# Kernel tuning notes

Hardware: AMD Instinct MI355X
Metric: run time of the kernel (lower is better)

Reference implementation:

```python
import jax, jax.numpy as jnp
import numpy as np

# --- HairBundle model constants (from init_kwargs: params + force_params) ---
# Nadrowski/Martin-style hair-bundle model with 5 state variables:
#   x_hb (bundle position), x_a (adaptation motor), p_m, p_gs, p_t (Ca probs)
LAM    = 1.0    # bundle friction
LAM_A  = 10.0   # adaptation-motor friction
K_GS   = 0.75   # gating-spring stiffness
K_SP   = 0.6    # stereociliary-pivot stiffness
K_ES   = 0.45   # extent spring stiffness
D_GATE = 0.5    # gating swing
DELTA  = 0.25   # channel sensitivity length
F_MAX  = 0.35   # max motor force
S_CA   = 0.9    # Ca feedback strength on motors
C_M    = 1.2    # Ca binding rate (motor site)
K_M    = 0.8    # Ca unbinding rate (motor site)
TAU_M  = 1.0
C_GS   = 0.7    # Ca binding rate (gating-spring site)
K_GSR  = 0.5    # Ca unbinding rate (gating-spring site)
TAU_GS = 1.0
C_T    = 0.3    # Ca binding rate (transduction site)
K_T    = 0.4    # Ca unbinding rate (transduction site)
TAU_T  = 1.0
HB_NOISE = 0.05 # diffusion on x_hb
A_NOISE  = 0.02 # diffusion on x_a
# force_params: sinusoidal driving force
F_AMP   = 0.5
F_OMEGA = 6.283185307179586
F_PHASE = 0.0

BATCH = 8_000_000  # number of SDE sample paths
NVARS = 5


def setup_inputs() -> dict:
    key = jax.random.key(0)
    k1, k2 = jax.random.split(key)
    t = jax.random.uniform(k1, (1,), dtype=jnp.float32)
    x = jax.random.normal(k2, (BATCH, NVARS), dtype=jnp.float32)
    return {"t": t, "x": x}


def reference(t, x):
    """Vectorized drift f(t, x) of the hair-bundle SDE (replaces the
    per-row python loop + sympy lambdified scalar evaluation) plus the
    constant diagonal diffusion g(t, x). Returns (drift, diffusion)."""
    x_hb, x_a, p_m, p_gs, p_t = (x[..., 0], x[..., 1], x[..., 2], x[..., 3], x[..., 4])

    # channel open probability and gating-spring force (elementwise, fused)
    p_o = jax.nn.sigmoid((x_hb - x_a) / DELTA)          # [B]
    f_gs = K_GS * (x_hb - x_a - D_GATE * p_o)           # [B]

    force = F_AMP * jnp.sin(F_OMEGA * t[0] + F_PHASE)   # scalar sin drive, added to dx_hb

    dx_hb = (-f_gs - K_SP * x_hb) / LAM + force
    dx_a  = (f_gs - K_ES * x_a - F_MAX * (1.0 - S_CA * p_m)) / LAM_A
    dp_m  = (C_M * p_o * (1.0 - p_m) - K_M * p_m) / TAU_M
    dp_gs = (C_GS * p_o * (1.0 - p_gs) - K_GSR * p_gs) / TAU_GS
    dp_t  = (C_T * p_o * (1.0 - p_t) - K_T * p_t) / TAU_T

    drift = jnp.stack([dx_hb, dx_a, dp_m, dp_gs, dp_t], axis=-1)  # [B, 5]

    # g: constant per-variable noise amplitudes tiled over the batch
    dsigma = jnp.array([HB_NOISE, A_NOISE, 0.0, 0.0, 0.0], dtype=x.dtype)
    diffusion = jnp.broadcast_to(dsigma, x.shape)  # [B, 5]

    return drift, diffusion
```

## Files before the change

### kernel.cpp

```cpp
#include <hip/hip_runtime.h>
#include <math.h>


__global__ __launch_bounds__(256) void hb_sde_kernel(
    const float* __restrict__ t,
    const float* __restrict__ x,
    float* __restrict__ out,
    int n_groups,
    long long batch)
{
    const long long tid = (long long)blockIdx.x * blockDim.x + threadIdx.x;
    if (tid >= n_groups) return;

    const float force = 0.5f * sinf(6.283185307179586f * t[0] + 0.0f);

    const float4* __restrict__ xv = (const float4*)x + tid * 5;
    float in[20];
    ((float4*)in)[0] = xv[0];
    ((float4*)in)[1] = xv[1];
    ((float4*)in)[2] = xv[2];
    ((float4*)in)[3] = xv[3];
    ((float4*)in)[4] = xv[4];

    float o[20];
#pragma unroll
    for (int r = 0; r < 4; ++r) {
        const float x_hb = in[r*5+0];
        const float x_a  = in[r*5+1];
        const float p_m  = in[r*5+2];
        const float p_gs = in[r*5+3];
        const float p_t  = in[r*5+4];

        const float p_o  = 1.0f / (1.0f + __expf(-4.0f * (x_hb - x_a)));
        const float f_gs = 0.75f * (x_hb - x_a - 0.5f * p_o);

        o[r*5+0] = -f_gs - 0.6f * x_hb + force;
        o[r*5+1] = 0.1f * (f_gs - 0.45f * x_a - 0.35f * (1.0f - 0.9f * p_m));
        o[r*5+2] = 1.2f * p_o * (1.0f - p_m)  - 0.8f * p_m;
        o[r*5+3] = 0.7f * p_o * (1.0f - p_gs) - 0.5f * p_gs;
        o[r*5+4] = 0.3f * p_o * (1.0f - p_t)  - 0.4f * p_t;
    }

    float4* __restrict__ dv = (float4*)out + tid * 5;
    dv[0] = ((float4*)o)[0];
    dv[1] = ((float4*)o)[1];
    dv[2] = ((float4*)o)[2];
    dv[3] = ((float4*)o)[3];
    dv[4] = ((float4*)o)[4];

    float4* __restrict__ gv = (float4*)(out + batch * 5) + tid * 5;
    gv[0] = make_float4(0.05f, 0.02f, 0.0f,  0.0f);
    gv[1] = make_float4(0.0f,  0.05f, 0.02f, 0.0f);
    gv[2] = make_float4(0.0f,  0.0f,  0.05f, 0.02f);
    gv[3] = make_float4(0.0f,  0.0f,  0.0f,  0.05f);
    gv[4] = make_float4(0.02f, 0.0f,  0.0f,  0.0f);
}

extern "C" void kernel_launch(void* const* d_in, const int* in_sizes, int n_in,
                              void* d_out, int out_size, void* d_ws, size_t ws_size,
                              hipStream_t stream) {
    const float* t = (const float*)d_in[0];
    const float* x = (const float*)d_in[1];
    float* out = (float*)d_out;

    const long long batch = (long long)in_sizes[1] / 5;
    const int n_groups = (int)(batch / 4);

    const int block = 256;
    const int grid = (n_groups + block - 1) / block;
    hb_sde_kernel<<<grid, block, 0, stream>>>(t, x, out, n_groups, batch);
}
```

Baseline: 456.5 us.

## Stage rows through LDS for coalesced float4 loads and nontemporal stores

Each block cooperatively loads 512 rows as contiguous float4s into shared memory, computes the drift in place, then writes drift and the constant diffusion pattern back with coalesced nontemporal stores. This replaces per-thread 80-byte-strided vector accesses that poorly coalesce. It adds LDS traffic and two barriers, uses smaller blocks, and drops the tail bounds check, assuming batch is a multiple of 512.

```diff
diff --git a/kernel.cpp b/kernel.cpp
--- a/kernel.cpp
+++ b/kernel.cpp
@@ -2,58 +2,70 @@
 #include <math.h>
 
 
-__global__ __launch_bounds__(256) void hb_sde_kernel(
+typedef float f4 __attribute__((ext_vector_type(4)));
+
+#define THREADS        128
+#define ROWS_PER_BLOCK 512
+#define F4_PER_BLOCK   (ROWS_PER_BLOCK * 5 / 4)
+#define F4_PER_THREAD  (F4_PER_BLOCK / THREADS)
+#define ROWS_PER_THREAD (ROWS_PER_BLOCK / THREADS)
+
+__global__ __launch_bounds__(THREADS) void hb_sde_kernel(
     const float* __restrict__ t,
     const float* __restrict__ x,
-    float* __restrict__ out,
-    int n_groups,
-    long long batch)
+    float* __restrict__ drift,
+    float* __restrict__ diff)
 {
-    const long long tid = (long long)blockIdx.x * blockDim.x + threadIdx.x;
-    if (tid >= n_groups) return;
+    __shared__ float lds[ROWS_PER_BLOCK * 5];
 
-    const float force = 0.5f * sinf(6.283185307179586f * t[0] + 0.0f);
+    const int i = threadIdx.x;
+    const long long f4base = (long long)blockIdx.x * F4_PER_BLOCK;
 
-    const float4* __restrict__ xv = (const float4*)x + tid * 5;
-    float in[20];
-    ((float4*)in)[0] = xv[0];
-    ((float4*)in)[1] = xv[1];
-    ((float4*)in)[2] = xv[2];
-    ((float4*)in)[3] = xv[3];
-    ((float4*)in)[4] = xv[4];
+    const float force = 0.5f * sinf(6.283185307179586f * t[0]);
 
-    float o[20];
+    const f4* __restrict__ xv = (const f4*)x + f4base;
+    f4* lv = (f4*)lds;
 #pragma unroll
-    for (int r = 0; r < 4; ++r) {
-        const float x_hb = in[r*5+0];
-        const float x_a  = in[r*5+1];
-        const float p_m  = in[r*5+2];
-        const float p_gs = in[r*5+3];
-        const float p_t  = in[r*5+4];
+    for (int k = 0; k < F4_PER_THREAD; ++k)
+        lv[i + k * THREADS] = __builtin_nontemporal_load(&xv[i + k * THREADS]);
+    __syncthreads();
+
+#pragma unroll
+    for (int r = 0; r < ROWS_PER_THREAD; ++r) {
+        const int o = (i * ROWS_PER_THREAD + r) * 5;
+        const float x_hb = lds[o + 0];
+        const float x_a  = lds[o + 1];
+        const float p_m  = lds[o + 2];
+        const float p_gs = lds[o + 3];
+        const float p_t  = lds[o + 4];
 
         const float p_o  = 1.0f / (1.0f + __expf(-4.0f * (x_hb - x_a)));
         const float f_gs = 0.75f * (x_hb - x_a - 0.5f * p_o);
 
-        o[r*5+0] = -f_gs - 0.6f * x_hb + force;
-        o[r*5+1] = 0.1f * (f_gs - 0.45f * x_a - 0.35f * (1.0f - 0.9f * p_m));
-        o[r*5+2] = 1.2f * p_o * (1.0f - p_m)  - 0.8f * p_m;
-        o[r*5+3] = 0.7f * p_o * (1.0f - p_gs) - 0.5f * p_gs;
-        o[r*5+4] = 0.3f * p_o * (1.0f - p_t)  - 0.4f * p_t;
+        lds[o + 0] = -f_gs - 0.6f * x_hb + force;
+        lds[o + 1] = 0.1f * (f_gs - 0.45f * x_a - 0.35f * (1.0f - 0.9f * p_m));
+        lds[o + 2] = 1.2f * p_o * (1.0f - p_m)  - 0.8f * p_m;
+        lds[o + 3] = 0.7f * p_o * (1.0f - p_gs) - 0.5f * p_gs;
+        lds[o + 4] = 0.3f * p_o * (1.0f - p_t)  - 0.4f * p_t;
     }
+    __syncthreads();
 
-    float4* __restrict__ dv = (float4*)out + tid * 5;
-    dv[0] = ((float4*)o)[0];
-    dv[1] = ((float4*)o)[1];
-    dv[2] = ((float4*)o)[2];
-    dv[3] = ((float4*)o)[3];
-    dv[4] = ((float4*)o)[4];
+    f4* __restrict__ dv = (f4*)drift + f4base;
+#pragma unroll
+    for (int k = 0; k < F4_PER_THREAD; ++k)
+        __builtin_nontemporal_store(lv[i + k * THREADS], &dv[i + k * THREADS]);
 
-    float4* __restrict__ gv = (float4*)(out + batch * 5) + tid * 5;
-    gv[0] = make_float4(0.05f, 0.02f, 0.0f,  0.0f);
-    gv[1] = make_float4(0.0f,  0.05f, 0.02f, 0.0f);
-    gv[2] = make_float4(0.0f,  0.0f,  0.05f, 0.02f);
-    gv[3] = make_float4(0.0f,  0.0f,  0.0f,  0.05f);
-    gv[4] = make_float4(0.02f, 0.0f,  0.0f,  0.0f);
+    f4* __restrict__ gv = (f4*)diff + f4base;
+#pragma unroll
+    for (int k = 0; k < F4_PER_THREAD; ++k) {
+        const int m = (i + k * THREADS) % 5;
+        f4 v;
+        v.x = (m == 0) ? 0.05f : ((m == 4) ? 0.02f : 0.0f);
+        v.y = (m == 0) ? 0.02f : ((m == 1) ? 0.05f : 0.0f);
+        v.z = (m == 1) ? 0.02f : ((m == 2) ? 0.05f : 0.0f);
+        v.w = (m == 2) ? 0.02f : ((m == 3) ? 0.05f : 0.0f);
+        __builtin_nontemporal_store(v, &gv[i + k * THREADS]);
+    }
 }
 
 extern "C" void kernel_launch(void* const* d_in, const int* in_sizes, int n_in,
@@ -64,9 +76,9 @@
     float* out = (float*)d_out;
 
     const long long batch = (long long)in_sizes[1] / 5;
-    const int n_groups = (int)(batch / 4);
+    float* drift = out;
+    float* diff  = out + batch * 5;
 
-    const int block = 256;
-    const int grid = (n_groups + block - 1) / block;
-    hb_sde_kernel<<<grid, block, 0, stream>>>(t, x, out, n_groups, batch);
+    const int nblocks = (int)(batch / ROWS_PER_BLOCK);
+    hb_sde_kernel<<<nblocks, THREADS, 0, stream>>>(t, x, drift, diff);
 }
```

New measurement: 410.9 us. 1.11x faster.

## Switch to one-thread-per-element coalesced access with nontemporal stores

Applied to the files above, without the earlier changes.

Replaces the four-rows-per-thread float4 scheme, whose accesses were strided by 80 bytes per lane, with one thread per output element. Each thread reloads its row's shared fields, so adjacent lanes read and write consecutive addresses. Drift and diffusion stores use nontemporal hints. The cost is redundant loads and recomputation of the sigmoid for every element, plus more threads and per-element index division.

```diff
diff --git a/kernel.cpp b/kernel.cpp
--- a/kernel.cpp
+++ b/kernel.cpp
@@ -2,58 +2,43 @@
 #include <math.h>
 
 
-__global__ __launch_bounds__(256) void hb_sde_kernel(
+#define THREADS 256
+
+__global__ __launch_bounds__(THREADS) void hb_sde_kernel(
     const float* __restrict__ t,
     const float* __restrict__ x,
-    float* __restrict__ out,
-    int n_groups,
-    long long batch)
+    float* __restrict__ drift,
+    float* __restrict__ diff,
+    unsigned n)
 {
-    const long long tid = (long long)blockIdx.x * blockDim.x + threadIdx.x;
-    if (tid >= n_groups) return;
+    const unsigned j = blockIdx.x * THREADS + threadIdx.x;
+    if (j >= n) return;
 
-    const float force = 0.5f * sinf(6.283185307179586f * t[0] + 0.0f);
+    const float force = 0.5f * sinf(6.283185307179586f * t[0]);
 
-    const float4* __restrict__ xv = (const float4*)x + tid * 5;
-    float in[20];
-    ((float4*)in)[0] = xv[0];
-    ((float4*)in)[1] = xv[1];
-    ((float4*)in)[2] = xv[2];
-    ((float4*)in)[3] = xv[3];
-    ((float4*)in)[4] = xv[4];
+    const unsigned r = j / 5u;
+    const unsigned v = j - r * 5u;
+    const unsigned b = r * 5u;
 
-    float o[20];
-#pragma unroll
-    for (int r = 0; r < 4; ++r) {
-        const float x_hb = in[r*5+0];
-        const float x_a  = in[r*5+1];
-        const float p_m  = in[r*5+2];
-        const float p_gs = in[r*5+3];
-        const float p_t  = in[r*5+4];
+    const float x_hb = x[b + 0];
+    const float x_a  = x[b + 1];
+    const float p_m  = x[b + 2];
+    const float p_v  = x[j];
 
-        const float p_o  = 1.0f / (1.0f + __expf(-4.0f * (x_hb - x_a)));
-        const float f_gs = 0.75f * (x_hb - x_a - 0.5f * p_o);
+    const float p_o  = 1.0f / (1.0f + __expf(-4.0f * (x_hb - x_a)));
+    const float f_gs = 0.75f * (x_hb - x_a - 0.5f * p_o);
 
-        o[r*5+0] = -f_gs - 0.6f * x_hb + force;
-        o[r*5+1] = 0.1f * (f_gs - 0.45f * x_a - 0.35f * (1.0f - 0.9f * p_m));
-        o[r*5+2] = 1.2f * p_o * (1.0f - p_m)  - 0.8f * p_m;
-        o[r*5+3] = 0.7f * p_o * (1.0f - p_gs) - 0.5f * p_gs;
-        o[r*5+4] = 0.3f * p_o * (1.0f - p_t)  - 0.4f * p_t;
-    }
+    const float d0 = -f_gs - 0.6f * x_hb + force;
+    const float d1 = 0.1f * (f_gs - 0.45f * x_a - 0.35f * (1.0f - 0.9f * p_m));
+    const float a  = (v == 2) ? 1.2f : ((v == 3) ? 0.7f : 0.3f);
+    const float k  = (v == 2) ? 0.8f : ((v == 3) ? 0.5f : 0.4f);
+    const float d2 = a * p_o * (1.0f - p_v) - k * p_v;
 
-    float4* __restrict__ dv = (float4*)out + tid * 5;
-    dv[0] = ((float4*)o)[0];
-    dv[1] = ((float4*)o)[1];
-    dv[2] = ((float4*)o)[2];
-    dv[3] = ((float4*)o)[3];
-    dv[4] = ((float4*)o)[4];
+    const float d = (v == 0) ? d0 : ((v == 1) ? d1 : d2);
+    __builtin_nontemporal_store(d, &drift[j]);
 
-    float4* __restrict__ gv = (float4*)(out + batch * 5) + tid * 5;
-    gv[0] = make_float4(0.05f, 0.02f, 0.0f,  0.0f);
-    gv[1] = make_float4(0.0f,  0.05f, 0.02f, 0.0f);
-    gv[2] = make_float4(0.0f,  0.0f,  0.05f, 0.02f);
-    gv[3] = make_float4(0.0f,  0.0f,  0.0f,  0.05f);
-    gv[4] = make_float4(0.02f, 0.0f,  0.0f,  0.0f);
+    const float g = (v == 0) ? 0.05f : ((v == 1) ? 0.02f : 0.0f);
+    __builtin_nontemporal_store(g, &diff[j]);
 }
 
 extern "C" void kernel_launch(void* const* d_in, const int* in_sizes, int n_in,
@@ -63,10 +48,10 @@
     const float* x = (const float*)d_in[1];
     float* out = (float*)d_out;
 
-    const long long batch = (long long)in_sizes[1] / 5;
-    const int n_groups = (int)(batch / 4);
+    const unsigned n = (unsigned)in_sizes[1];
+    float* drift = out;
+    float* diff  = out + (size_t)n;
 
-    const int block = 256;
-    const int grid = (n_groups + block - 1) / block;
-    hb_sde_kernel<<<grid, block, 0, stream>>>(t, x, out, n_groups, batch);
+    const int grid = (int)((n + THREADS - 1) / THREADS);
+    hb_sde_kernel<<<grid, THREADS, 0, stream>>>(t, x, drift, diff, n);
 }
```

After: 481.5 us. +5.5%, slower.
